# Performance work log

Measured on AMD Instinct MI355X. Metric: run time of the kernel, lower is better.

## Reference

```python
import jax, jax.numpy as jnp
import numpy as np

EPS = 1e-5
BN_GAMMA = 1.0
BN_BETA = 1e-4  # per torch init: BN weight=1, bias=0.0001


def bn(h):
    # BatchNorm1d in training mode: biased batch variance
    mu = h.mean(axis=0)
    var = h.var(axis=0)
    return (h - mu) * (BN_GAMMA / jnp.sqrt(var + EPS)) + BN_BETA


def gcn_conv(h, W, b, row, col, n, edge_weight=None):
    # PyG-style GCNConv: linear -> add self loops (w=1) -> sym deg norm -> scatter-sum
    h = h @ W
    e = row.shape[0]
    ew = jnp.ones((e,), h.dtype) if edge_weight is None else edge_weight
    loop = jnp.arange(n, dtype=row.dtype)
    r = jnp.concatenate([row, loop])
    c = jnp.concatenate([col, loop])
    w = jnp.concatenate([ew, jnp.ones((n,), h.dtype)])
    deg = jax.ops.segment_sum(w, r, num_segments=n)
    dinv = jnp.where(deg > 0, jax.lax.rsqrt(deg + jnp.where(deg > 0, 0.0, 1.0)), 0.0)
    norm = dinv[r] * w * dinv[c]  # [E+N]
    msg = h[r] * norm[:, None]    # gather + per-edge scale
    out = jax.ops.segment_sum(msg, c, num_segments=n)  # scatter-aggregate
    return out + b


def readout(h, W1, b1, W2, b2):
    h = bn(h) @ W1 + b1
    h = bn(jax.nn.relu(h)) @ W2 + b2
    return jax.nn.log_softmax(h, axis=-1)


def setup_inputs() -> dict:
    key = jax.random.key(0)
    ks = jax.random.split(key, 12)
    N, E, F, H, C = 50000, 800000, 128, 128, 10
    s = 0.05
    return {
        "x": jax.random.normal(ks[0], (N, F), jnp.float32),
        "edge_index": jax.random.randint(ks[1], (2, E), 0, N, jnp.int32),
        "perm": jax.random.permutation(ks[2], N).astype(jnp.int32),
        "W_feat": jax.random.normal(ks[3], (F, H), jnp.float32) * s,
        "b_feat": jnp.zeros((H,), jnp.float32),
        "W_convs": jax.random.normal(ks[4], (3, H, H), jnp.float32) * s,
        "b_convs": jnp.zeros((3, H), jnp.float32),
        "W_ea": jax.random.normal(ks[5], (2 * H, 2), jnp.float32) * s,
        "b_ea": jnp.zeros((2,), jnp.float32),
        "W_na": jax.random.normal(ks[6], (H, 2), jnp.float32) * s,
        "b_na": jnp.zeros((2,), jnp.float32),
        "W_ctx": jax.random.normal(ks[7], (H, H), jnp.float32) * s,
        "b_ctx": jnp.zeros((H,), jnp.float32),
        "W_obj": jax.random.normal(ks[8], (H, H), jnp.float32) * s,
        "b_obj": jnp.zeros((H,), jnp.float32),
        "W_fc1": jax.random.normal(ks[9], (3, H, H), jnp.float32) * s,  # c,o,co
        "b_fc1": jnp.zeros((3, H), jnp.float32),
        "W_fc2": jax.random.normal(ks[10], (3, H, C), jnp.float32) * s,
        "b_fc2": jnp.zeros((3, C), jnp.float32),
    }


def reference(x, edge_index, perm, W_feat, b_feat, W_convs, b_convs, W_ea, b_ea,
              W_na, b_na, W_ctx, b_ctx, W_obj, b_obj, W_fc1, b_fc1, W_fc2, b_fc2):
    n = x.shape[0]
    row, col = edge_index[0], edge_index[1]
    h = bn(x)
    h = jax.nn.relu(h @ W_feat + b_feat)  # conv_feat has gfn=True -> pure linear
    for i in range(3):
        h = jax.nn.relu(gcn_conv(bn(h), W_convs[i], b_convs[i], row, col, n))
    edge_rep = jnp.concatenate([h[row], h[col]], axis=-1)  # [E, 2H]
    edge_att = jax.nn.softmax(edge_rep @ W_ea + b_ea, axis=-1)
    node_att = jax.nn.softmax(h @ W_na + b_na, axis=-1)
    xc = node_att[:, 0:1] * h
    xo = node_att[:, 1:2] * h
    xc = jax.nn.relu(gcn_conv(bn(xc), W_ctx, b_ctx, row, col, n, edge_att[:, 0]))
    xo = jax.nn.relu(gcn_conv(bn(xo), W_obj, b_obj, row, col, n, edge_att[:, 1]))
    xc_logis = readout(xc, W_fc1[0], b_fc1[0], W_fc2[0], b_fc2[0])
    xo_logis = readout(xo, W_fc1[1], b_fc1[1], W_fc2[1], b_fc2[1])
    xco_logis = readout(xc[perm] + xo, W_fc1[2], b_fc1[2], W_fc2[2], b_fc2[2])
    return (xc_logis, xo_logis, xco_logis)
```

## Files before the change

kernel.cpp:

```cpp
#include <hip/hip_runtime.h>
#include <math.h>

#define H 128
#define NCLS 10
#define EPS 1e-5f
#define BN_BETA 1e-4f
#define CS_BLOCKS 256

typedef unsigned short u16;
typedef unsigned int u32;
typedef __attribute__((ext_vector_type(8))) short short8;
typedef __attribute__((ext_vector_type(4))) float floatx4;

__device__ inline float bflo(u32 u) { union { u32 i; float f; } a; a.i = u << 16; return a.f; }
__device__ inline float bfhi(u32 u) { union { u32 i; float f; } a; a.i = u & 0xffff0000u; return a.f; }
__device__ inline u16 f2bf(float f) {
  union { float f; u32 i; } v; v.f = f;
  return (u16)((v.i + 0x7fff + ((v.i >> 16) & 1)) >> 16);
}
__device__ inline u32 pack2(float a, float b) { return (u32)f2bf(a) | ((u32)f2bf(b) << 16); }

__device__ inline void reduce_partials(const float* __restrict__ P, int nb, int stride,
                                       int off0, int f, float* su_out, float* sq_out) {
  float su[8] = {0, 0, 0, 0, 0, 0, 0, 0}, sq[8] = {0, 0, 0, 0, 0, 0, 0, 0};
  int b = 0;
  for (; b + 8 <= nb; b += 8) {
#pragma unroll
    for (int u = 0; u < 8; u++) {
      const float* p = P + (size_t)(b + u) * stride + off0;
      su[u] += p[f];
      sq[u] += p[128 + f];
    }
  }
  for (; b < nb; b++) {
    const float* p = P + (size_t)b * stride + off0;
    su[0] += p[f];
    sq[0] += p[128 + f];
  }
  *su_out = ((su[0] + su[1]) + (su[2] + su[3])) + ((su[4] + su[5]) + (su[6] + su[7]));
  *sq_out = ((sq[0] + sq[1]) + (sq[2] + sq[3])) + ((sq[4] + sq[5]) + (sq[6] + sq[7]));
}

__global__ __launch_bounds__(256) void xstats_kernel(
    const float* __restrict__ x, int n4, float* __restrict__ stp) {
  int tid = threadIdx.x;
  int lane = tid & 63, wave = tid >> 6;
  float s[4] = {0, 0, 0, 0}, q[4] = {0, 0, 0, 0};
  int step = gridDim.x * 256;
  for (int i = blockIdx.x * 256 + tid; i < n4; i += step) {
    float4 v = ((const float4*)x)[i];
    s[0] += v.x; q[0] += v.x * v.x; s[1] += v.y; q[1] += v.y * v.y;
    s[2] += v.z; q[2] += v.z * v.z; s[3] += v.w; q[3] += v.w * v.w;
  }
#pragma unroll
  for (int k = 0; k < 4; k++) { s[k] += __shfl_xor(s[k], 32); q[k] += __shfl_xor(q[k], 32); }
  __shared__ float sm[4][256];
  int col = (lane & 31) * 4;
  if (lane < 32) {
#pragma unroll
    for (int k = 0; k < 4; k++) { sm[wave][col + k] = s[k]; sm[wave][128 + col + k] = q[k]; }
  }
  __syncthreads();
  stp[(size_t)blockIdx.x * 256 + tid] = sm[0][tid] + sm[1][tid] + sm[2][tid] + sm[3][tid];
}

__global__ __launch_bounds__(256) void colstats_kernel(
    const u16* __restrict__ X, int N, float* __restrict__ stp) {
  int tid = threadIdx.x;
  int li = tid & 15, rg = tid >> 4;
  int wave = tid >> 6, lane = tid & 63;
  const uint4* T = (const uint4*)X;
  float s[8] = {0, 0, 0, 0, 0, 0, 0, 0}, q[8] = {0, 0, 0, 0, 0, 0, 0, 0};
  for (int r = blockIdx.x * 16 + rg; r < N; r += CS_BLOCKS * 16) {
    uint4 u = T[(size_t)r * 16 + li];
    float f[8] = {bflo(u.x), bfhi(u.x), bflo(u.y), bfhi(u.y),
                  bflo(u.z), bfhi(u.z), bflo(u.w), bfhi(u.w)};
#pragma unroll
    for (int j = 0; j < 8; j++) { s[j] += f[j]; q[j] += f[j] * f[j]; }
  }
#pragma unroll
  for (int j = 0; j < 8; j++) {
    s[j] += __shfl_xor(s[j], 16); s[j] += __shfl_xor(s[j], 32);
    q[j] += __shfl_xor(q[j], 16); q[j] += __shfl_xor(q[j], 32);
  }
  __shared__ float sm[4][256];
  if ((lane & 48) == 0) {
#pragma unroll
    for (int j = 0; j < 8; j++) {
      sm[wave][li * 8 + j] = s[j];
      sm[wave][128 + li * 8 + j] = q[j];
    }
  }
  __syncthreads();
  stp[(size_t)blockIdx.x * 256 + tid] = sm[0][tid] + sm[1][tid] + sm[2][tid] + sm[3][tid];
}

__device__ inline void fold_body(const float* P, int nb, int stride, int off0,
                                 const float* W, const float* bias,
                                 float invN, int k, u16* Wt, float* cf) {
  int f = threadIdx.x;
  float su, sq;
  reduce_partials(P, nb, stride, off0, f, &su, &sq);
  float mu = su * invN;
  float var = sq * invN - mu * mu;
  float s = 1.0f / sqrtf(fmaxf(var, 0.f) + EPS);
  float w = W[(size_t)f * H + k];
  Wt[(size_t)k * H + f] = f2bf(s * w);
  __shared__ float red[H];
  red[f] = (BN_BETA - mu * s) * w;
  __syncthreads();
  for (int o = 64; o > 0; o >>= 1) {
    if (f < o) red[f] += red[f + o];
    __syncthreads();
  }
  if (f == 0) cf[k] = red[0] + (bias ? bias[k] : 0.f);
}

__global__ __launch_bounds__(128) void fold_kernel(
    const float* P, int nb, const float* W, const float* bias, float invN,
    u16* Wt, float* cf) {
  fold_body(P, nb, 256, 0, W, bias, invN, blockIdx.x, Wt, cf);
}

__global__ __launch_bounds__(128) void fold2_kernel(
    const float* P, int nb, const float* W0, const float* W1, float invN,
    u16* Wt2, float* cf2) {
  int j = blockIdx.x >> 7, k = blockIdx.x & 127;
  fold_body(P, nb, 512, j * 256, j ? W1 : W0, nullptr, invN, k,
            Wt2 + (size_t)j * H * H, cf2 + j * H);
}

__global__ __launch_bounds__(128) void fold3_kernel(
    const float* PC, int nbC, const float* PO, int nbO, const float* PCO, int nbCO,
    const float* W_fc1, const float* b_fc1, float invN, u16* Wt3, float* cf3) {
  int j = blockIdx.x >> 7, k = blockIdx.x & 127;
  const float* P = (j == 0) ? PC : (j == 1) ? PO : PCO;
  int nb = (j == 0) ? nbC : (j == 1) ? nbO : nbCO;
  fold_body(P, nb, 256, 0, W_fc1 + (size_t)j * H * H, b_fc1 + j * H, invN, k,
            Wt3 + (size_t)j * H * H, cf3 + j * H);
}

__global__ __launch_bounds__(128) void fold10x3_kernel(
    const float* stpZ, int nb, const float* W_fc2, const float* b_fc2, float invN,
    float* W2f, float* c2f) {
  int j = blockIdx.x / NCLS, k = blockIdx.x % NCLS;
  const float* P = stpZ + (size_t)j * nb * 256;
  int f = threadIdx.x;
  float su, sq;
  reduce_partials(P, nb, 256, 0, f, &su, &sq);
  float mu = su * invN;
  float var = sq * invN - mu * mu;
  float s = 1.0f / sqrtf(fmaxf(var, 0.f) + EPS);
  float w = W_fc2[(size_t)j * H * NCLS + (size_t)f * NCLS + k];
  W2f[(size_t)j * H * NCLS + (size_t)f * NCLS + k] = s * w;
  __shared__ float red[H];
  red[f] = (BN_BETA - mu * s) * w;
  __syncthreads();
  for (int o = 64; o > 0; o >>= 1) {
    if (f < o) red[f] += red[f + o];
    __syncthreads();
  }
  if (f == 0) c2f[j * 16 + k] = red[0] + b_fc2[j * NCLS + k];
}

__device__ inline void gemm_core(const u16* A, const float* Afp, const u16* Bt,
                                 const float* cf, const float* b2, const float* sumw,
                                 u16* C, int N, int relu, int blk, float* stp) {
  int tid = threadIdx.x;
  int wave = tid >> 6, lane = tid & 63;
  int l15 = lane & 15, quad = lane >> 4;
  int row0 = (blk * 4 + wave) * 16;
  if (row0 >= N && !stp) return;
  int arow = row0 + l15;
  short8 a[4];
  short8 z8 = {0, 0, 0, 0, 0, 0, 0, 0};
  if (Afp) {
#pragma unroll
    for (int k4 = 0; k4 < 4; k4++) {
      if (arow < N) {
        const float* p = Afp + (size_t)arow * H + k4 * 32 + quad * 8;
        float4 f0 = *(const float4*)p;
        float4 f1 = *(const float4*)(p + 4);
        union { short8 s8; u32 u[4]; } cv;
        cv.u[0] = pack2(f0.x, f0.y); cv.u[1] = pack2(f0.z, f0.w);
        cv.u[2] = pack2(f1.x, f1.y); cv.u[3] = pack2(f1.z, f1.w);
        a[k4] = cv.s8;
      } else a[k4] = z8;
    }
  } else {
#pragma unroll
    for (int k4 = 0; k4 < 4; k4++)
      a[k4] = (arow < N) ? *(const short8*)(A + (size_t)arow * H + k4 * 32 + quad * 8) : z8;
  }
  float srow[4];
  if (sumw) {
#pragma unroll
    for (int r = 0; r < 4; r++) {
      int row = row0 + quad * 4 + r;
      srow[r] = (row < N) ? sumw[row] : 0.f;
    }
  }
  float ps[8], pq[8];
#pragma unroll
  for (int nt = 0; nt < 8; nt++) {
    floatx4 acc = {0.f, 0.f, 0.f, 0.f};
    const u16* bp = Bt + (size_t)(nt * 16 + l15) * H + quad * 8;
#pragma unroll
    for (int k4 = 0; k4 < 4; k4++) {
      short8 b = *(const short8*)(bp + k4 * 32);
      acc = __builtin_amdgcn_mfma_f32_16x16x32_bf16(a[k4], b, acc, 0, 0, 0);
    }
    int col = nt * 16 + l15;
    float base = cf[col];
    float bb = b2 ? b2[col] : 0.f;
    float s_ = 0.f, q_ = 0.f;
#pragma unroll
    for (int r = 0; r < 4; r++) {
      int row = row0 + quad * 4 + r;
      if (row < N) {
        float v = acc[r] + (sumw ? srow[r] * base + bb : base);
        if (relu) v = fmaxf(v, 0.f);
        s_ += v; q_ += v * v;
        C[(size_t)row * H + col] = f2bf(v);
      }
    }
    ps[nt] = s_; pq[nt] = q_;
  }
  if (stp) {
    __shared__ float sred[4][256];
#pragma unroll
    for (int nt = 0; nt < 8; nt++) {
      ps[nt] += __shfl_xor(ps[nt], 16); ps[nt] += __shfl_xor(ps[nt], 32);
      pq[nt] += __shfl_xor(pq[nt], 16); pq[nt] += __shfl_xor(pq[nt], 32);
    }
    if (quad == 0) {
#pragma unroll
      for (int nt = 0; nt < 8; nt++) {
        sred[wave][nt * 16 + l15] = ps[nt];
        sred[wave][128 + nt * 16 + l15] = pq[nt];
      }
    }
    __syncthreads();
    stp[(size_t)blk * 256 + tid] =
        sred[0][tid] + sred[1][tid] + sred[2][tid] + sred[3][tid];
  }
}

__global__ __launch_bounds__(256) void gemm_kernel(
    const u16* A, const u16* Bt, const float* cf, u16* C, int N, int relu) {
  gemm_core(A, nullptr, Bt, cf, nullptr, nullptr, C, N, relu, blockIdx.x, nullptr);
}

__global__ __launch_bounds__(256) void gemm_x_kernel(
    const float* x, const u16* Bt, const float* cf, u16* C, int N, float* stp) {
  gemm_core(nullptr, x, Bt, cf, nullptr, nullptr, C, N, 1, blockIdx.x, stp);
}

__global__ __launch_bounds__(256) void gemm2sw_kernel(
    u16* B0, u16* B1, const u16* Wt2, const float* cf2,
    const float* b0, const float* b1, const float* sw0, const float* sw1,
    int N, int gG, float* stp) {
  int j = blockIdx.x / gG, blk = blockIdx.x % gG;
  u16* Z = j ? B1 : B0;
  gemm_core(Z, nullptr, Wt2 + (size_t)j * H * H, cf2 + j * H, j ? b1 : b0,
            j ? sw1 : sw0, Z, N, 1, blk, stp + (size_t)j * gG * 256);
}

__global__ __launch_bounds__(256) void gemm3_kernel(
    u16* Z0, u16* Z1, u16* Z2, const u16* Wt3, const float* cf3,
    int N, int gG, float* stp) {
  int j = blockIdx.x / gG, blk = blockIdx.x % gG;
  u16* Z = (j == 0) ? Z0 : (j == 1) ? Z1 : Z2;
  gemm_core(Z, nullptr, Wt3 + (size_t)j * H * H, cf3 + j * H, nullptr, nullptr,
            Z, N, 1, blk, stp + (size_t)j * gG * 256);
}

__global__ __launch_bounds__(256) void hist_kernel(
    const int* __restrict__ row, const int* __restrict__ col, int E,
    int* __restrict__ cnt, float* __restrict__ deg) {
  int e = blockIdx.x * 256 + threadIdx.x;
  if (e < E) {
    atomicAdd(&cnt[col[e]], 1);
    atomicAdd(&deg[row[e]], 1.0f);
  }
}

__global__ __launch_bounds__(256) void scanA_rsqrt_kernel(
    const int* __restrict__ cnt, const float* __restrict__ deg, int N,
    int* __restrict__ partial, float* __restrict__ dinv) {
  int i = blockIdx.x * 256 + threadIdx.x;
  if (i < N) dinv[i] = 1.0f / sqrtf(deg[i] + 1.0f);
  __shared__ int sd[256];
  sd[threadIdx.x] = (i < N) ? cnt[i] : 0;
  __syncthreads();
  for (int o = 128; o > 0; o >>= 1) {
    if (threadIdx.x < o) sd[threadIdx.x] += sd[threadIdx.x + o];
    __syncthreads();
  }
  if (threadIdx.x == 0) partial[blockIdx.x] = sd[0];
}

__global__ __launch_bounds__(256) void scanB_kernel(const int* __restrict__ partial, int nb,
                                                    int* __restrict__ blockoff) {
  __shared__ int sd[256];
  int t = threadIdx.x;
  int v = (t < nb) ? partial[t] : 0;
  sd[t] = v;
  __syncthreads();
  for (int o = 1; o < 256; o <<= 1) {
    int x = (t >= o) ? sd[t - o] : 0;
    __syncthreads();
    sd[t] += x;
    __syncthreads();
  }
  blockoff[t] = sd[t] - v;
}

__global__ __launch_bounds__(256) void scanC_kernel(
    const int* __restrict__ cnt, int N, const int* __restrict__ blockoff,
    int* __restrict__ off, int* __restrict__ cur, int E) {
  __shared__ int sd[256];
  int t = threadIdx.x;
  int i = blockIdx.x * 256 + t;
  int v = (i < N) ? cnt[i] : 0;
  sd[t] = v;
  __syncthreads();
  for (int o = 1; o < 256; o <<= 1) {
    int x = (t >= o) ? sd[t - o] : 0;
    __syncthreads();
    sd[t] += x;
    __syncthreads();
  }
  if (i < N) {
    int ex = blockoff[blockIdx.x] + sd[t] - v;
    off[i] = ex;
    cur[i] = ex;
  }
  if (i == 0) off[N] = E;
}

__global__ __launch_bounds__(256) void place_kernel(
    const int* __restrict__ row, const int* __restrict__ col, int E,
    int* __restrict__ cur, const float* __restrict__ dinv,
    int* __restrict__ csr_src, int* __restrict__ slot_of, float* __restrict__ wn) {
  int e = blockIdx.x * 256 + threadIdx.x;
  if (e < E) {
    int r = row[e];
    int slot = atomicAdd(&cur[col[e]], 1);
    csr_src[slot] = r;
    slot_of[e] = slot;
    wn[slot] = dinv[r];
  }
}

__global__ __launch_bounds__(256) void rsqrt2_kernel(
    const float* __restrict__ deg, const float* __restrict__ degc,
    float* __restrict__ dinvc, float* __restrict__ dinvo, int N) {
  int v = blockIdx.x * 256 + threadIdx.x;
  if (v < N) {
    float dc = degc[v];
    dinvc[v] = 1.0f / sqrtf(dc + 1.0f);
    dinvo[v] = 1.0f / sqrtf(deg[v] - dc + 1.0f);
  }
}

__global__ __launch_bounds__(256) void wa2_kernel(
    const int* csr_src, float* att_and_wa0r, const float* dinvc, const float* dinvo,
    const float2* na01, float* wa0n, float* wa1n, float* wa1r, int E) {
  int i = blockIdx.x * 256 + threadIdx.x;
  if (i >= E) return;
  int s = csr_src[i];
  float a0 = att_and_wa0r[i];
  float2 na = na01[s];
  float r0 = a0 * dinvc[s];
  float r1 = (1.0f - a0) * dinvo[s];
  wa0n[i] = r0 * na.x;
  wa1n[i] = r1 * na.y;
  att_and_wa0r[i] = r0;
  wa1r[i] = r1;
}

#define ACC8(A, U, W)                                             \
  A[0] += (W) * bflo(U.x); A[1] += (W) * bfhi(U.x);               \
  A[2] += (W) * bflo(U.y); A[3] += (W) * bfhi(U.y);               \
  A[4] += (W) * bflo(U.z); A[5] += (W) * bfhi(U.z);               \
  A[6] += (W) * bflo(U.w); A[7] += (W) * bfhi(U.w);

__global__ __launch_bounds__(256) void agg_kernel(
    const u16* __restrict__ t, const int* __restrict__ csr_src,
    const float* __restrict__ wseg, const int* __restrict__ off,
    const float* __restrict__ dinv, const float* __restrict__ bias,
    u16* __restrict__ out, int N) {
  int v = blockIdx.x * 4 + (threadIdx.x >> 6);
  if (v >= N) return;
  int lane = threadIdx.x & 63;
  int g = lane >> 4, li = lane & 15;
  const uint4* T = (const uint4*)t;
  float dv = dinv[v];
  float acc[8] = {0.f, 0.f, 0.f, 0.f, 0.f, 0.f, 0.f, 0.f};
  if (g == 0) {
    uint4 u = T[(size_t)v * 16 + li];
    float w0 = dv * dv;
    ACC8(acc, u, w0)
  }
  int s0 = off[v], s1 = off[v + 1];
  for (int s = s0; s < s1; s += 32) {
    int ix[8]; float wv[8];
#pragma unroll
    for (int u = 0; u < 8; u++) {
      int e = s + g + u * 4;
      bool ok = e < s1;
      int e2 = ok ? e : s0;
      ix[u] = csr_src[e2];
      wv[u] = ok ? wseg[e2] : 0.f;
    }
    uint4 uu[8];
#pragma unroll
    for (int u = 0; u < 8; u++) uu[u] = T[(size_t)ix[u] * 16 + li];
#pragma unroll
    for (int u = 0; u < 8; u++) { float w = wv[u] * dv; ACC8(acc, uu[u], w) }
  }
#pragma unroll
  for (int j = 0; j < 8; j++) {
    acc[j] += __shfl_xor(acc[j], 16);
    acc[j] += __shfl_xor(acc[j], 32);
  }
  if (g == 0) {
    float o[8];
#pragma unroll
    for (int j = 0; j < 8; j++) o[j] = fmaxf(acc[j] + bias[li * 8 + j], 0.f);
    uint4 w4;
    w4.x = pack2(o[0], o[1]); w4.y = pack2(o[2], o[3]);
    w4.z = pack2(o[4], o[5]); w4.w = pack2(o[6], o[7]);
    ((uint4*)out)[(size_t)v * 16 + li] = w4;
  }
}

__global__ __launch_bounds__(256) void aggdual_kernel(
    const u16* __restrict__ h, const int* __restrict__ csr_src,
    const float* __restrict__ wa0n, const float* __restrict__ wa1n,
    const float* __restrict__ wa0r, const float* __restrict__ wa1r,
    const int* __restrict__ off, const float* __restrict__ dinvc,
    const float* __restrict__ dinvo, const float2* __restrict__ na01,
    u16* __restrict__ gc, u16* __restrict__ go,
    float* __restrict__ sumw_c, float* __restrict__ sumw_o, int N) {
  int v = blockIdx.x * 4 + (threadIdx.x >> 6);
  if (v >= N) return;
  int lane = threadIdx.x & 63;
  int g = lane >> 4, li = lane & 15;
  const uint4* T = (const uint4*)h;
  float dvc = dinvc[v], dvo = dinvo[v];
  float ac[8] = {0.f, 0.f, 0.f, 0.f, 0.f, 0.f, 0.f, 0.f};
  float ao[8] = {0.f, 0.f, 0.f, 0.f, 0.f, 0.f, 0.f, 0.f};
  float swc = 0.f, swo = 0.f;
  if (g == 0) {
    uint4 u = T[(size_t)v * 16 + li];
    float2 na = na01[v];
    float wc = dvc * dvc, wo = dvo * dvo;
    float wch = wc * na.x, woh = wo * na.y;
    ACC8(ac, u, wch)
    ACC8(ao, u, woh)
  }
  int s0 = off[v], s1 = off[v + 1];
  for (int s = s0; s < s1; s += 16) {
    int ix[4]; float w0n[4], w1n[4], w0r[4], w1r[4];
#pragma unroll
    for (int u = 0; u < 4; u++) {
      int e = s + g + u * 4;
      bool ok = e < s1;
      int e2 = ok ? e : s0;
      ix[u] = csr_src[e2];
      w0n[u] = ok ? wa0n[e2] : 0.f;
      w1n[u] = ok ? wa1n[e2] : 0.f;
      w0r[u] = ok ? wa0r[e2] : 0.f;
      w1r[u] = ok ? wa1r[e2] : 0.f;
    }
    uint4 uu[4];
#pragma unroll
    for (int u = 0; u < 4; u++) uu[u] = T[(size_t)ix[u] * 16 + li];
#pragma unroll
    for (int u = 0; u < 4; u++) {
      float wc = w0n[u] * dvc; ACC8(ac, uu[u], wc)
      float wo = w1n[u] * dvo; ACC8(ao, uu[u], wo)
      swc += w0r[u]; swo += w1r[u];
    }
  }
#pragma unroll
  for (int j = 0; j < 8; j++) {
    ac[j] += __shfl_xor(ac[j], 16); ac[j] += __shfl_xor(ac[j], 32);
    ao[j] += __shfl_xor(ao[j], 16); ao[j] += __shfl_xor(ao[j], 32);
  }
  swc += __shfl_xor(swc, 16); swc += __shfl_xor(swc, 32);
  swo += __shfl_xor(swo, 16); swo += __shfl_xor(swo, 32);
  if (g == 0) {
    uint4 wc4, wo4;
    wc4.x = pack2(ac[0], ac[1]); wc4.y = pack2(ac[2], ac[3]);
    wc4.z = pack2(ac[4], ac[5]); wc4.w = pack2(ac[6], ac[7]);
    wo4.x = pack2(ao[0], ao[1]); wo4.y = pack2(ao[2], ao[3]);
    wo4.z = pack2(ao[4], ao[5]); wo4.w = pack2(ao[6], ao[7]);
    ((uint4*)gc)[(size_t)v * 16 + li] = wc4;
    ((uint4*)go)[(size_t)v * 16 + li] = wo4;
    if (li == 0) {
      sumw_c[v] = dvc * swc + dvc * dvc;
      sumw_o[v] = dvo * swo + dvo * dvo;
    }
  }
}

__global__ __launch_bounds__(256) void natt_kernel(
    const u16* __restrict__ h, int N,
    const float* __restrict__ W_na, const float* __restrict__ b_na,
    const float* __restrict__ W_ea,
    float2* __restrict__ na01, float2* __restrict__ p01, float2* __restrict__ q01) {
  int n = blockIdx.x * 256 + threadIdx.x;
  if (n >= N) return;
  float sa0 = 0, sa1 = 0, sp0 = 0, sp1 = 0, sq0 = 0, sq1 = 0;
  const uint2* hr = (const uint2*)(h + (size_t)n * H);
  for (int c = 0; c < 32; c++) {
    uint2 u = hr[c];
    float v0 = bflo(u.x), v1 = bfhi(u.x), v2 = bflo(u.y), v3 = bfhi(u.y);
    int k = c * 4;
    sa0 += v0 * W_na[k * 2] + v1 * W_na[k * 2 + 2] + v2 * W_na[k * 2 + 4] + v3 * W_na[k * 2 + 6];
    sa1 += v0 * W_na[k * 2 + 1] + v1 * W_na[k * 2 + 3] + v2 * W_na[k * 2 + 5] + v3 * W_na[k * 2 + 7];
    sp0 += v0 * W_ea[k * 2] + v1 * W_ea[k * 2 + 2] + v2 * W_ea[k * 2 + 4] + v3 * W_ea[k * 2 + 6];
    sp1 += v0 * W_ea[k * 2 + 1] + v1 * W_ea[k * 2 + 3] + v2 * W_ea[k * 2 + 5] + v3 * W_ea[k * 2 + 7];
    sq0 += v0 * W_ea[(H + k) * 2] + v1 * W_ea[(H + k) * 2 + 2] + v2 * W_ea[(H + k) * 2 + 4] + v3 * W_ea[(H + k) * 2 + 6];
    sq1 += v0 * W_ea[(H + k) * 2 + 1] + v1 * W_ea[(H + k) * 2 + 3] + v2 * W_ea[(H + k) * 2 + 5] + v3 * W_ea[(H + k) * 2 + 7];
  }
  sa0 += b_na[0]; sa1 += b_na[1];
  float m = fmaxf(sa0, sa1);
  float e0 = expf(sa0 - m), e1 = expf(sa1 - m);
  float inv = 1.f / (e0 + e1);
  na01[n] = make_float2(e0 * inv, e1 * inv);
  p01[n] = make_float2(sp0, sp1);
  q01[n] = make_float2(sq0, sq1);
}

__global__ __launch_bounds__(256) void xprestats_kernel(
    const u16* __restrict__ h, const float2* __restrict__ na01, int n4,
    float* __restrict__ stp) {
  int tid = threadIdx.x;
  int lane = tid & 63, wave = tid >> 6;
  float sc[4] = {0, 0, 0, 0}, qc[4] = {0, 0, 0, 0};
  float so[4] = {0, 0, 0, 0}, qo[4] = {0, 0, 0, 0};
  int step = gridDim.x * 256;
  for (int i = blockIdx.x * 256 + tid; i < n4; i += step) {
    int n = i >> 5;
    uint2 u = ((const uint2*)h)[i];
    float v0 = bflo(u.x), v1 = bfhi(u.x), v2 = bflo(u.y), v3 = bfhi(u.y);
    float2 ab = na01[n];
    float a = ab.x, b = ab.y;
    float c0 = v0 * a, c1 = v1 * a, c2 = v2 * a, c3 = v3 * a;
    float o0 = v0 * b, o1 = v1 * b, o2 = v2 * b, o3 = v3 * b;
    sc[0] += c0; qc[0] += c0 * c0; sc[1] += c1; qc[1] += c1 * c1;
    sc[2] += c2; qc[2] += c2 * c2; sc[3] += c3; qc[3] += c3 * c3;
    so[0] += o0; qo[0] += o0 * o0; so[1] += o1; qo[1] += o1 * o1;
    so[2] += o2; qo[2] += o2 * o2; so[3] += o3; qo[3] += o3 * o3;
  }
#pragma unroll
  for (int k = 0; k < 4; k++) {
    sc[k] += __shfl_xor(sc[k], 32); qc[k] += __shfl_xor(qc[k], 32);
    so[k] += __shfl_xor(so[k], 32); qo[k] += __shfl_xor(qo[k], 32);
  }
  __shared__ float sm[4][512];
  int col = (lane & 31) * 4;
  if (lane < 32) {
#pragma unroll
    for (int k = 0; k < 4; k++) {
      sm[wave][col + k] = sc[k];
      sm[wave][128 + col + k] = qc[k];
      sm[wave][256 + col + k] = so[k];
      sm[wave][384 + col + k] = qo[k];
    }
  }
  __syncthreads();
  float r0 = sm[0][tid] + sm[1][tid] + sm[2][tid] + sm[3][tid];
  float r1 = sm[0][256 + tid] + sm[1][256 + tid] + sm[2][256 + tid] + sm[3][256 + tid];
  stp[(size_t)blockIdx.x * 512 + tid] = r0;
  stp[(size_t)blockIdx.x * 512 + 256 + tid] = r1;
}

__global__ __launch_bounds__(256) void eatt_kernel(
    const int* __restrict__ row, const int* __restrict__ col, int E,
    const float2* __restrict__ p01, const float2* __restrict__ q01,
    const float* __restrict__ b_ea, const int* __restrict__ slot_of,
    float* __restrict__ att0s, float* __restrict__ degc) {
  int e = blockIdx.x * 256 + threadIdx.x;
  if (e >= E) return;
  int r = row[e], c = col[e];
  float2 p = p01[r], q = q01[c];
  float l0 = p.x + q.x + b_ea[0];
  float l1 = p.y + q.y + b_ea[1];
  float a0 = 1.0f / (1.0f + expf(l1 - l0));
  att0s[slot_of[e]] = a0;
  atomicAdd(&degc[r], a0);
}

__global__ __launch_bounds__(256) void permadd_stats_kernel(
    const u16* __restrict__ xc, const u16* __restrict__ xo,
    const int* __restrict__ perm, u16* __restrict__ out, int n4, float* __restrict__ stp) {
  int tid = threadIdx.x;
  int lane = tid & 63, wave = tid >> 6;
  float s[4] = {0, 0, 0, 0}, q[4] = {0, 0, 0, 0};
  int step = gridDim.x * 256;
  for (int i = blockIdx.x * 256 + tid; i < n4; i += step) {
    int n = i >> 5, k = i & 31;
    int p = perm[n];
    uint2 a = ((const uint2*)xc)[(size_t)p * 32 + k];
    uint2 b = ((const uint2*)xo)[i];
    float f0 = bflo(a.x) + bflo(b.x), f1 = bfhi(a.x) + bfhi(b.x);
    float f2 = bflo(a.y) + bflo(b.y), f3 = bfhi(a.y) + bfhi(b.y);
    ((uint2*)out)[i] = make_uint2(pack2(f0, f1), pack2(f2, f3));
    s[0] += f0; q[0] += f0 * f0; s[1] += f1; q[1] += f1 * f1;
    s[2] += f2; q[2] += f2 * f2; s[3] += f3; q[3] += f3 * f3;
  }
#pragma unroll
  for (int k = 0; k < 4; k++) { s[k] += __shfl_xor(s[k], 32); q[k] += __shfl_xor(q[k], 32); }
  __shared__ float sm[4][256];
  int col = (lane & 31) * 4;
  if (lane < 32) {
#pragma unroll
    for (int k = 0; k < 4; k++) { sm[wave][col + k] = s[k]; sm[wave][128 + col + k] = q[k]; }
  }
  __syncthreads();
  stp[(size_t)blockIdx.x * 256 + tid] = sm[0][tid] + sm[1][tid] + sm[2][tid] + sm[3][tid];
}

__global__ __launch_bounds__(256) void fc2x3_kernel(
    const u16* __restrict__ z0, const u16* __restrict__ z1, const u16* __restrict__ z2,
    const float* __restrict__ W2f, const float* __restrict__ c2f,
    float* __restrict__ outp, int N, int gN) {
  int j = blockIdx.x / gN, blk = blockIdx.x % gN;
  int n = blk * 256 + threadIdx.x;
  if (n >= N) return;
  const u16* z = (j == 0) ? z0 : (j == 1) ? z1 : z2;
  const float* W2 = W2f + (size_t)j * H * NCLS;
  const float* c2 = c2f + j * 16;
  float* op = outp + (size_t)j * N * NCLS;
  float acc[NCLS];
#pragma unroll
  for (int c = 0; c < NCLS; c++) acc[c] = c2[c];
  const uint2* zr = (const uint2*)(z + (size_t)n * H);
  for (int c4 = 0; c4 < 32; c4++) {
    uint2 u = zr[c4];
    float v[4] = {bflo(u.x), bfhi(u.x), bflo(u.y), bfhi(u.y)};
    int k = c4 * 4;
#pragma unroll
    for (int jj = 0; jj < 4; jj++)
#pragma unroll
      for (int c = 0; c < NCLS; c++) acc[c] += v[jj] * W2[(k + jj) * NCLS + c];
  }
  float m = acc[0];
#pragma unroll
  for (int c = 1; c < NCLS; c++) m = fmaxf(m, acc[c]);
  float s = 0.f;
#pragma unroll
  for (int c = 0; c < NCLS; c++) s += expf(acc[c] - m);
  float lse = logf(s) + m;
#pragma unroll
  for (int c = 0; c < NCLS; c++) op[(size_t)n * NCLS + c] = acc[c] - lse;
}

extern "C" void kernel_launch(void* const* d_in, const int* in_sizes, int n_in,
                              void* d_out, int out_size, void* d_ws, size_t ws_size,
                              hipStream_t stream) {
  const int N = in_sizes[0] / H;
  const int E = in_sizes[1] / 2;
  const float* x = (const float*)d_in[0];
  const int* ei = (const int*)d_in[1];
  const int* row = ei;
  const int* col = ei + E;
  const int* perm = (const int*)d_in[2];
  const float* W_feat = (const float*)d_in[3];
  const float* b_feat = (const float*)d_in[4];
  const float* W_convs = (const float*)d_in[5];
  const float* b_convs = (const float*)d_in[6];
  const float* W_ea = (const float*)d_in[7];
  const float* b_ea = (const float*)d_in[8];
  const float* W_na = (const float*)d_in[9];
  const float* b_na = (const float*)d_in[10];
  const float* W_ctx = (const float*)d_in[11];
  const float* b_ctx = (const float*)d_in[12];
  const float* W_obj = (const float*)d_in[13];
  const float* b_obj = (const float*)d_in[14];
  const float* W_fc1 = (const float*)d_in[15];
  const float* b_fc1 = (const float*)d_in[16];
  const float* W_fc2 = (const float*)d_in[17];
  const float* b_fc2 = (const float*)d_in[18];
  float* out = (float*)d_out;

  const int gG = (N + 63) / 64;
  const int gN = (N + 255) / 256;
  const int gE = (E + 255) / 256;
  const int SB = (N + 255) / 256;
  const int n4 = N * 32;
  const int gAgg = (N + 3) / 4;
  const float invN = 1.0f / (float)N;

  char* base = (char*)d_ws;
  size_t off_b = 0;
  auto alloc = [&](size_t bytes) -> void* {
    void* p = base + off_b;
    off_b = (off_b + bytes + 255) & ~(size_t)255;
    return p;
  };
  size_t NB2 = (size_t)N * H * sizeof(u16);
  u16* bufA = (u16*)alloc(NB2);
  u16* bufB = (u16*)alloc(NB2);
  u16* bufC = (u16*)alloc(NB2);
  u16* bufD = (u16*)alloc(NB2);
  int* cnt = (int*)alloc(3 * (size_t)N * 4);
  float* deg = (float*)(cnt + N);
  float* degc = (float*)(cnt + 2 * (size_t)N);
  float* stpX = (float*)alloc((size_t)CS_BLOCKS * 256 * 4);
  float* stpG = (float*)alloc(3 * (size_t)gG * 256 * 4);
  float* stpPre = (float*)alloc((size_t)CS_BLOCKS * 512 * 4);
  float* stpCO = (float*)alloc((size_t)CS_BLOCKS * 256 * 4);
  int* off = (int*)alloc(((size_t)N + 1) * 4);
  int* cur = (int*)alloc((size_t)N * 4);
  float* dinv = (float*)alloc((size_t)N * 4);
  float* dinvc = (float*)alloc((size_t)N * 4);
  float* dinvo = (float*)alloc((size_t)N * 4);
  float* sumw_c = (float*)alloc((size_t)N * 4);
  float* sumw_o = (float*)alloc((size_t)N * 4);
  float2* na01 = (float2*)alloc((size_t)N * 8);
  float2* p01 = (float2*)alloc((size_t)N * 8);
  float2* q01 = (float2*)alloc((size_t)N * 8);
  int* partial = (int*)alloc(256 * 4);
  int* blockoff = (int*)alloc(256 * 4);
  u16* Wt = (u16*)alloc((size_t)H * H * 2);
  u16* Wt2 = (u16*)alloc(2 * (size_t)H * H * 2);
  u16* Wt3 = (u16*)alloc(3 * (size_t)H * H * 2);
  float* cf = (float*)alloc(H * 4);
  float* cf2 = (float*)alloc(2 * H * 4);
  float* cf3 = (float*)alloc(3 * H * 4);
  float* W2f = (float*)alloc(3 * (size_t)H * NCLS * 4);
  float* c2f = (float*)alloc(3 * 16 * 4);
  int* csr_src = (int*)alloc((size_t)E * 4);
  int* slot_of = (int*)alloc((size_t)E * 4);
  float* att0s = (float*)alloc((size_t)E * 4);
  float* wn = (float*)alloc((size_t)E * 4);
  float* waX = (float*)alloc((size_t)E * 4);
  float* wa0n = (float*)slot_of;
  float* wa1n = wn;
  float* wa0r = att0s;
  float* wa1r = waX;

  hipMemsetAsync(cnt, 0, 3 * (size_t)N * 4, stream);

  hist_kernel<<<gE, 256, 0, stream>>>(row, col, E, cnt, deg);
  scanA_rsqrt_kernel<<<SB, 256, 0, stream>>>(cnt, deg, N, partial, dinv);
  scanB_kernel<<<1, 256, 0, stream>>>(partial, SB, blockoff);
  scanC_kernel<<<SB, 256, 0, stream>>>(cnt, N, blockoff, off, cur, E);
  place_kernel<<<gE, 256, 0, stream>>>(row, col, E, cur, dinv, csr_src, slot_of, wn);

  xstats_kernel<<<CS_BLOCKS, 256, 0, stream>>>(x, n4, stpX);
  fold_kernel<<<H, H, 0, stream>>>(stpX, CS_BLOCKS, W_feat, b_feat, invN, Wt, cf);
  gemm_x_kernel<<<gG, 256, 0, stream>>>(x, Wt, cf, bufA, N, stpG);

  const float* stprev = stpG;
  int nbprev = gG;
  for (int i = 0; i < 3; ++i) {
    fold_kernel<<<H, H, 0, stream>>>(stprev, nbprev, W_convs + (size_t)i * H * H,
                                     nullptr, invN, Wt, cf);
    gemm_kernel<<<gG, 256, 0, stream>>>(bufA, Wt, cf, bufB, N, 0);
    agg_kernel<<<gAgg, 256, 0, stream>>>(bufB, csr_src, wn, off, dinv,
                                         b_convs + (size_t)i * H, bufA, N);
    if (i < 2) {
      colstats_kernel<<<CS_BLOCKS, 256, 0, stream>>>(bufA, N, stpX);
      stprev = stpX; nbprev = CS_BLOCKS;
    }
  }

  natt_kernel<<<gN, 256, 0, stream>>>(bufA, N, W_na, b_na, W_ea, na01, p01, q01);
  eatt_kernel<<<gE, 256, 0, stream>>>(row, col, E, p01, q01, b_ea, slot_of, att0s, degc);
  rsqrt2_kernel<<<gN, 256, 0, stream>>>(deg, degc, dinvc, dinvo, N);
  wa2_kernel<<<gE, 256, 0, stream>>>(csr_src, att0s, dinvc, dinvo, na01,
                                     wa0n, wa1n, wa1r, E);
  xprestats_kernel<<<CS_BLOCKS, 256, 0, stream>>>(bufA, na01, n4, stpPre);

  fold2_kernel<<<2 * H, H, 0, stream>>>(stpPre, CS_BLOCKS, W_ctx, W_obj, invN, Wt2, cf2);
  aggdual_kernel<<<gAgg, 256, 0, stream>>>(bufA, csr_src, wa0n, wa1n, wa0r, wa1r,
                                           off, dinvc, dinvo, na01, bufC, bufD,
                                           sumw_c, sumw_o, N);
  gemm2sw_kernel<<<2 * gG, 256, 0, stream>>>(bufC, bufD, Wt2, cf2, b_ctx, b_obj,
                                             sumw_c, sumw_o, N, gG, stpG);

  permadd_stats_kernel<<<CS_BLOCKS, 256, 0, stream>>>(bufC, bufD, perm, bufA, n4, stpCO);

  fold3_kernel<<<3 * H, H, 0, stream>>>(stpG, gG, stpG + (size_t)gG * 256, gG,
                                        stpCO, CS_BLOCKS, W_fc1, b_fc1, invN, Wt3, cf3);
  gemm3_kernel<<<3 * gG, 256, 0, stream>>>(bufC, bufD, bufA, Wt3, cf3, N, gG, stpG);
  fold10x3_kernel<<<3 * NCLS, H, 0, stream>>>(stpG, gG, W_fc2, b_fc2, invN, W2f, c2f);
  fc2x3_kernel<<<3 * gN, 256, 0, stream>>>(bufC, bufD, bufA, W2f, c2f, out, N, gN);
}
```

Measured before the change: 920.0 us.

## Fuse independent small kernels into combined launches and fold rsqrt into edge weights

Pairs independent kernels (hist+xstats, scanA+fold, scanB+gemm_x, scanC+fold, place+gemm, eatt+xprestats, wa2+fold2) into single launches that split work by block index. This cuts the number of serial kernel launches and the idle gaps between dependent stages. The fold kernels now handle two output columns per 256-thread block. The rsqrt2 kernel is removed: wa2 computes the attention-degree normalisation inline and writes packed float2 weights for aggdual. The risk is heterogeneous blocks in one grid causing load imbalance, and extra edge-sized buffers.

```diff
diff --git a/kernel.cpp b/kernel.cpp
--- a/kernel.cpp
+++ b/kernel.cpp
@@ -41,64 +41,12 @@
   *sq_out = ((sq[0] + sq[1]) + (sq[2] + sq[3])) + ((sq[4] + sq[5]) + (sq[6] + sq[7]));
 }
 
-__global__ __launch_bounds__(256) void xstats_kernel(
-    const float* __restrict__ x, int n4, float* __restrict__ stp) {
-  int tid = threadIdx.x;
-  int lane = tid & 63, wave = tid >> 6;
-  float s[4] = {0, 0, 0, 0}, q[4] = {0, 0, 0, 0};
-  int step = gridDim.x * 256;
-  for (int i = blockIdx.x * 256 + tid; i < n4; i += step) {
-    float4 v = ((const float4*)x)[i];
-    s[0] += v.x; q[0] += v.x * v.x; s[1] += v.y; q[1] += v.y * v.y;
-    s[2] += v.z; q[2] += v.z * v.z; s[3] += v.w; q[3] += v.w * v.w;
-  }
-#pragma unroll
-  for (int k = 0; k < 4; k++) { s[k] += __shfl_xor(s[k], 32); q[k] += __shfl_xor(q[k], 32); }
-  __shared__ float sm[4][256];
-  int col = (lane & 31) * 4;
-  if (lane < 32) {
-#pragma unroll
-    for (int k = 0; k < 4; k++) { sm[wave][col + k] = s[k]; sm[wave][128 + col + k] = q[k]; }
-  }
-  __syncthreads();
-  stp[(size_t)blockIdx.x * 256 + tid] = sm[0][tid] + sm[1][tid] + sm[2][tid] + sm[3][tid];
-}
-
-__global__ __launch_bounds__(256) void colstats_kernel(
-    const u16* __restrict__ X, int N, float* __restrict__ stp) {
-  int tid = threadIdx.x;
-  int li = tid & 15, rg = tid >> 4;
-  int wave = tid >> 6, lane = tid & 63;
-  const uint4* T = (const uint4*)X;
-  float s[8] = {0, 0, 0, 0, 0, 0, 0, 0}, q[8] = {0, 0, 0, 0, 0, 0, 0, 0};
-  for (int r = blockIdx.x * 16 + rg; r < N; r += CS_BLOCKS * 16) {
-    uint4 u = T[(size_t)r * 16 + li];
-    float f[8] = {bflo(u.x), bfhi(u.x), bflo(u.y), bfhi(u.y),
-                  bflo(u.z), bfhi(u.z), bflo(u.w), bfhi(u.w)};
-#pragma unroll
-    for (int j = 0; j < 8; j++) { s[j] += f[j]; q[j] += f[j] * f[j]; }
-  }
-#pragma unroll
-  for (int j = 0; j < 8; j++) {
-    s[j] += __shfl_xor(s[j], 16); s[j] += __shfl_xor(s[j], 32);
-    q[j] += __shfl_xor(q[j], 16); q[j] += __shfl_xor(q[j], 32);
-  }
-  __shared__ float sm[4][256];
-  if ((lane & 48) == 0) {
-#pragma unroll
-    for (int j = 0; j < 8; j++) {
-      sm[wave][li * 8 + j] = s[j];
-      sm[wave][128 + li * 8 + j] = q[j];
-    }
-  }
-  __syncthreads();
-  stp[(size_t)blockIdx.x * 256 + tid] = sm[0][tid] + sm[1][tid] + sm[2][tid] + sm[3][tid];
-}
-
-__device__ inline void fold_body(const float* P, int nb, int stride, int off0,
-                                 const float* W, const float* bias,
-                                 float invN, int k, u16* Wt, float* cf) {
-  int f = threadIdx.x;
+__device__ inline void fold256_body(const float* P, int nb, int stride, int off0,
+                                    const float* W, const float* bias, float invN,
+                                    int kp, u16* Wt, float* cf) {
+  int f = threadIdx.x & 127;
+  int half = threadIdx.x >> 7;
+  int k = kp * 2 + half;
   float su, sq;
   reduce_partials(P, nb, stride, off0, f, &su, &sq);
   float mu = su * invN;
@@ -106,38 +54,351 @@
   float s = 1.0f / sqrtf(fmaxf(var, 0.f) + EPS);
   float w = W[(size_t)f * H + k];
   Wt[(size_t)k * H + f] = f2bf(s * w);
-  __shared__ float red[H];
-  red[f] = (BN_BETA - mu * s) * w;
+  __shared__ float red[2][128];
+  red[half][f] = (BN_BETA - mu * s) * w;
   __syncthreads();
   for (int o = 64; o > 0; o >>= 1) {
-    if (f < o) red[f] += red[f + o];
+    if (f < o) red[half][f] += red[half][f + o];
     __syncthreads();
   }
-  if (f == 0) cf[k] = red[0] + (bias ? bias[k] : 0.f);
-}
-
-__global__ __launch_bounds__(128) void fold_kernel(
+  if (f == 0) cf[k] = red[half][0] + (bias ? bias[k] : 0.f);
+}
+
+__device__ inline void hist_body(const int* __restrict__ row, const int* __restrict__ col,
+                                 int E, int* cnt, float* deg, int blk) {
+  int e = blk * 256 + threadIdx.x;
+  if (e < E) {
+    atomicAdd(&cnt[col[e]], 1);
+    atomicAdd(&deg[row[e]], 1.0f);
+  }
+}
+
+__device__ inline void xstats_body(const float* __restrict__ x, int n4,
+                                   float* __restrict__ stp, int blk) {
+  int tid = threadIdx.x;
+  int lane = tid & 63, wave = tid >> 6;
+  float s[4] = {0, 0, 0, 0}, q[4] = {0, 0, 0, 0};
+  int step = CS_BLOCKS * 256;
+  for (int i = blk * 256 + tid; i < n4; i += step) {
+    float4 v = ((const float4*)x)[i];
+    s[0] += v.x; q[0] += v.x * v.x; s[1] += v.y; q[1] += v.y * v.y;
+    s[2] += v.z; q[2] += v.z * v.z; s[3] += v.w; q[3] += v.w * v.w;
+  }
+#pragma unroll
+  for (int k = 0; k < 4; k++) { s[k] += __shfl_xor(s[k], 32); q[k] += __shfl_xor(q[k], 32); }
+  __shared__ float smx[4][256];
+  int col = (lane & 31) * 4;
+  if (lane < 32) {
+#pragma unroll
+    for (int k = 0; k < 4; k++) { smx[wave][col + k] = s[k]; smx[wave][128 + col + k] = q[k]; }
+  }
+  __syncthreads();
+  stp[(size_t)blk * 256 + tid] = smx[0][tid] + smx[1][tid] + smx[2][tid] + smx[3][tid];
+}
+
+__device__ inline void scanA_body(const int* cnt, const float* deg, int N,
+                                  int* partial, float* dinv, float* degc, int blk) {
+  int i = blk * 256 + threadIdx.x;
+  if (i < N) {
+    dinv[i] = 1.0f / sqrtf(deg[i] + 1.0f);
+    degc[i] = 0.f;
+  }
+  __shared__ int sdA[256];
+  sdA[threadIdx.x] = (i < N) ? cnt[i] : 0;
+  __syncthreads();
+  for (int o = 128; o > 0; o >>= 1) {
+    if (threadIdx.x < o) sdA[threadIdx.x] += sdA[threadIdx.x + o];
+    __syncthreads();
+  }
+  if (threadIdx.x == 0) partial[blk] = sdA[0];
+}
+
+__device__ inline void scanB_body(const int* partial, int nb, int* blockoff) {
+  __shared__ int sdB[256];
+  int t = threadIdx.x;
+  int v = (t < nb) ? partial[t] : 0;
+  sdB[t] = v;
+  __syncthreads();
+  for (int o = 1; o < 256; o <<= 1) {
+    int x = (t >= o) ? sdB[t - o] : 0;
+    __syncthreads();
+    sdB[t] += x;
+    __syncthreads();
+  }
+  blockoff[t] = sdB[t] - v;
+}
+
+__device__ inline void scanC_body(const int* cnt, int N, const int* blockoff,
+                                  int* off, int* cur, int E, int blk) {
+  __shared__ int sdC[256];
+  int t = threadIdx.x;
+  int i = blk * 256 + t;
+  int v = (i < N) ? cnt[i] : 0;
+  sdC[t] = v;
+  __syncthreads();
+  for (int o = 1; o < 256; o <<= 1) {
+    int x = (t >= o) ? sdC[t - o] : 0;
+    __syncthreads();
+    sdC[t] += x;
+    __syncthreads();
+  }
+  if (i < N) {
+    int ex = blockoff[blk] + sdC[t] - v;
+    off[i] = ex;
+    cur[i] = ex;
+  }
+  if (i == 0) off[N] = E;
+}
+
+__device__ inline void place_body(const int* row, const int* col, int E, int* cur,
+                                  const float* dinv, int* csr_src, int* slot_of,
+                                  float* wn, int blk) {
+  int e = blk * 256 + threadIdx.x;
+  if (e < E) {
+    int r = row[e];
+    int slot = atomicAdd(&cur[col[e]], 1);
+    csr_src[slot] = r;
+    slot_of[e] = slot;
+    wn[slot] = dinv[r];
+  }
+}
+
+__device__ inline void eatt_body(const int* row, const int* col, int E,
+                                 const float2* p01, const float2* q01,
+                                 const float* b_ea, const int* slot_of,
+                                 float* att0s, float* degc, int blk) {
+  int e = blk * 256 + threadIdx.x;
+  if (e >= E) return;
+  int r = row[e], c = col[e];
+  float2 p = p01[r], q = q01[c];
+  float l0 = p.x + q.x + b_ea[0];
+  float l1 = p.y + q.y + b_ea[1];
+  float a0 = 1.0f / (1.0f + expf(l1 - l0));
+  att0s[slot_of[e]] = a0;
+  atomicAdd(&degc[r], a0);
+}
+
+__device__ inline void xprestats_body(const u16* __restrict__ h,
+                                      const float2* __restrict__ na01, int n4,
+                                      float* __restrict__ stp, int blk) {
+  int tid = threadIdx.x;
+  int lane = tid & 63, wave = tid >> 6;
+  float sc[4] = {0, 0, 0, 0}, qc[4] = {0, 0, 0, 0};
+  float so[4] = {0, 0, 0, 0}, qo[4] = {0, 0, 0, 0};
+  int step = CS_BLOCKS * 256;
+  for (int i = blk * 256 + tid; i < n4; i += step) {
+    int n = i >> 5;
+    uint2 u = ((const uint2*)h)[i];
+    float v0 = bflo(u.x), v1 = bfhi(u.x), v2 = bflo(u.y), v3 = bfhi(u.y);
+    float2 ab = na01[n];
+    float a = ab.x, b = ab.y;
+    float c0 = v0 * a, c1 = v1 * a, c2 = v2 * a, c3 = v3 * a;
+    float o0 = v0 * b, o1 = v1 * b, o2 = v2 * b, o3 = v3 * b;
+    sc[0] += c0; qc[0] += c0 * c0; sc[1] += c1; qc[1] += c1 * c1;
+    sc[2] += c2; qc[2] += c2 * c2; sc[3] += c3; qc[3] += c3 * c3;
+    so[0] += o0; qo[0] += o0 * o0; so[1] += o1; qo[1] += o1 * o1;
+    so[2] += o2; qo[2] += o2 * o2; so[3] += o3; qo[3] += o3 * o3;
+  }
+#pragma unroll
+  for (int k = 0; k < 4; k++) {
+    sc[k] += __shfl_xor(sc[k], 32); qc[k] += __shfl_xor(qc[k], 32);
+    so[k] += __shfl_xor(so[k], 32); qo[k] += __shfl_xor(qo[k], 32);
+  }
+  __shared__ float smp[4][512];
+  int col = (lane & 31) * 4;
+  if (lane < 32) {
+#pragma unroll
+    for (int k = 0; k < 4; k++) {
+      smp[wave][col + k] = sc[k];
+      smp[wave][128 + col + k] = qc[k];
+      smp[wave][256 + col + k] = so[k];
+      smp[wave][384 + col + k] = qo[k];
+    }
+  }
+  __syncthreads();
+  float r0 = smp[0][tid] + smp[1][tid] + smp[2][tid] + smp[3][tid];
+  float r1 = smp[0][256 + tid] + smp[1][256 + tid] + smp[2][256 + tid] + smp[3][256 + tid];
+  stp[(size_t)blk * 512 + tid] = r0;
+  stp[(size_t)blk * 512 + 256 + tid] = r1;
+}
+
+__device__ inline void wa2_body(const int* csr_src, const float* att0s,
+                                const float* deg, const float* degc,
+                                const float2* na01, float2* wfa, float2* wfr,
+                                int E, int blk) {
+  int i = blk * 256 + threadIdx.x;
+  if (i >= E) return;
+  int s = csr_src[i];
+  float a0 = att0s[i];
+  float2 na = na01[s];
+  float dgc = degc[s];
+  float r0 = a0 / sqrtf(dgc + 1.0f);
+  float r1 = (1.0f - a0) / sqrtf(deg[s] - dgc + 1.0f);
+  wfa[i] = make_float2(r0 * na.x, r1 * na.y);
+  wfr[i] = make_float2(r0, r1);
+}
+
+__device__ inline void gemm_core(const u16* A, const float* Afp, const u16* Bt,
+                                 const float* cf, const float* b2, const float* sumw,
+                                 u16* C, int N, int relu, int blk, float* stp) {
+  int tid = threadIdx.x;
+  int wave = tid >> 6, lane = tid & 63;
+  int l15 = lane & 15, quad = lane >> 4;
+  int row0 = (blk * 4 + wave) * 16;
+  if (row0 >= N && !stp) return;
+  int arow = row0 + l15;
+  short8 a[4];
+  short8 z8 = {0, 0, 0, 0, 0, 0, 0, 0};
+  if (Afp) {
+#pragma unroll
+    for (int k4 = 0; k4 < 4; k4++) {
+      if (arow < N) {
+        const float* p = Afp + (size_t)arow * H + k4 * 32 + quad * 8;
+        float4 f0 = *(const float4*)p;
+        float4 f1 = *(const float4*)(p + 4);
+        union { short8 s8; u32 u[4]; } cv;
+        cv.u[0] = pack2(f0.x, f0.y); cv.u[1] = pack2(f0.z, f0.w);
+        cv.u[2] = pack2(f1.x, f1.y); cv.u[3] = pack2(f1.z, f1.w);
+        a[k4] = cv.s8;
+      } else a[k4] = z8;
+    }
+  } else {
+#pragma unroll
+    for (int k4 = 0; k4 < 4; k4++)
+      a[k4] = (arow < N) ? *(const short8*)(A + (size_t)arow * H + k4 * 32 + quad * 8) : z8;
+  }
+  float srow[4];
+  if (sumw) {
+#pragma unroll
+    for (int r = 0; r < 4; r++) {
+      int row = row0 + quad * 4 + r;
+      srow[r] = (row < N) ? sumw[row] : 0.f;
+    }
+  }
+  float ps[8], pq[8];
+#pragma unroll
+  for (int nt = 0; nt < 8; nt++) {
+    floatx4 acc = {0.f, 0.f, 0.f, 0.f};
+    const u16* bp = Bt + (size_t)(nt * 16 + l15) * H + quad * 8;
+#pragma unroll
+    for (int k4 = 0; k4 < 4; k4++) {
+      short8 b = *(const short8*)(bp + k4 * 32);
+      acc = __builtin_amdgcn_mfma_f32_16x16x32_bf16(a[k4], b, acc, 0, 0, 0);
+    }
+    int col = nt * 16 + l15;
+    float base = cf[col];
+    float bb = b2 ? b2[col] : 0.f;
+    float s_ = 0.f, q_ = 0.f;
+#pragma unroll
+    for (int r = 0; r < 4; r++) {
+      int row = row0 + quad * 4 + r;
+      if (row < N) {
+        float v = acc[r] + (sumw ? srow[r] * base + bb : base);
+        if (relu) v = fmaxf(v, 0.f);
+        s_ += v; q_ += v * v;
+        C[(size_t)row * H + col] = f2bf(v);
+      }
+    }
+    ps[nt] = s_; pq[nt] = q_;
+  }
+  if (stp) {
+    __shared__ float sred[4][256];
+#pragma unroll
+    for (int nt = 0; nt < 8; nt++) {
+      ps[nt] += __shfl_xor(ps[nt], 16); ps[nt] += __shfl_xor(ps[nt], 32);
+      pq[nt] += __shfl_xor(pq[nt], 16); pq[nt] += __shfl_xor(pq[nt], 32);
+    }
+    if (quad == 0) {
+#pragma unroll
+      for (int nt = 0; nt < 8; nt++) {
+        sred[wave][nt * 16 + l15] = ps[nt];
+        sred[wave][128 + nt * 16 + l15] = pq[nt];
+      }
+    }
+    __syncthreads();
+    stp[(size_t)blk * 256 + tid] =
+        sred[0][tid] + sred[1][tid] + sred[2][tid] + sred[3][tid];
+  }
+}
+
+__global__ __launch_bounds__(256) void hist_xstats_kernel(
+    const int* row, const int* col, int E, int* cnt, float* deg, int gE,
+    const float* x, int n4, float* stpX) {
+  if ((int)blockIdx.x < gE) hist_body(row, col, E, cnt, deg, blockIdx.x);
+  else xstats_body(x, n4, stpX, blockIdx.x - gE);
+}
+
+__global__ __launch_bounds__(256) void scanA_fold_kernel(
+    const int* cnt, const float* deg, int N, int* partial, float* dinv, float* degc,
+    int SB, const float* stpX, const float* W_feat, const float* b_feat, float invN,
+    u16* WtA, float* cfA) {
+  if ((int)blockIdx.x < SB) scanA_body(cnt, deg, N, partial, dinv, degc, blockIdx.x);
+  else fold256_body(stpX, CS_BLOCKS, 256, 0, W_feat, b_feat, invN, blockIdx.x - SB, WtA, cfA);
+}
+
+__global__ __launch_bounds__(256) void scanB_gemmx_kernel(
+    const int* partial, int nb, int* blockoff,
+    const float* x, const u16* WtA, const float* cfA, u16* C, int N, float* stpG) {
+  if (blockIdx.x == 0) scanB_body(partial, nb, blockoff);
+  else gemm_core(nullptr, x, WtA, cfA, nullptr, nullptr, C, N, 1, blockIdx.x - 1, stpG);
+}
+
+__global__ __launch_bounds__(256) void scanC_fold_kernel(
+    const int* cnt, int N, const int* blockoff, int* off, int* cur, int E, int SB,
+    const float* stpG, int nbG, const float* Wc, float invN, u16* WtB, float* cfB) {
+  if ((int)blockIdx.x < SB) scanC_body(cnt, N, blockoff, off, cur, E, blockIdx.x);
+  else fold256_body(stpG, nbG, 256, 0, Wc, nullptr, invN, blockIdx.x - SB, WtB, cfB);
+}
+
+__global__ __launch_bounds__(256) void place_gemm_kernel(
+    const int* row, const int* col, int E, int* cur, const float* dinv,
+    int* csr_src, int* slot_of, float* wn, int gE,
+    const u16* A, const u16* WtB, const float* cfB, u16* C, int N) {
+  if ((int)blockIdx.x < gE)
+    place_body(row, col, E, cur, dinv, csr_src, slot_of, wn, blockIdx.x);
+  else
+    gemm_core(A, nullptr, WtB, cfB, nullptr, nullptr, C, N, 0, blockIdx.x - gE, nullptr);
+}
+
+__global__ __launch_bounds__(256) void eatt_xpre_kernel(
+    const int* row, const int* col, int E, const float2* p01, const float2* q01,
+    const float* b_ea, const int* slot_of, float* att0s, float* degc, int gE,
+    const u16* h, const float2* na01, int n4, float* stpPre) {
+  if ((int)blockIdx.x < gE)
+    eatt_body(row, col, E, p01, q01, b_ea, slot_of, att0s, degc, blockIdx.x);
+  else
+    xprestats_body(h, na01, n4, stpPre, blockIdx.x - gE);
+}
+
+__global__ __launch_bounds__(256) void wa2_fold2_kernel(
+    const int* csr_src, const float* att0s, const float* deg, const float* degc,
+    const float2* na01, float2* wfa, float2* wfr, int E, int gE,
+    const float* stpPre, const float* W_ctx, const float* W_obj, float invN,
+    u16* Wt2, float* cf2) {
+  if ((int)blockIdx.x < gE)
+    wa2_body(csr_src, att0s, deg, degc, na01, wfa, wfr, E, blockIdx.x);
+  else {
+    int b = blockIdx.x - gE;
+    int j = b >> 6, kp = b & 63;
+    fold256_body(stpPre, CS_BLOCKS, 512, j * 256, j ? W_obj : W_ctx, nullptr, invN, kp,
+                 Wt2 + (size_t)j * H * H, cf2 + j * H);
+  }
+}
+
+__global__ __launch_bounds__(256) void fold256_kernel(
     const float* P, int nb, const float* W, const float* bias, float invN,
     u16* Wt, float* cf) {
-  fold_body(P, nb, 256, 0, W, bias, invN, blockIdx.x, Wt, cf);
-}
-
-__global__ __launch_bounds__(128) void fold2_kernel(
-    const float* P, int nb, const float* W0, const float* W1, float invN,
-    u16* Wt2, float* cf2) {
-  int j = blockIdx.x >> 7, k = blockIdx.x & 127;
-  fold_body(P, nb, 512, j * 256, j ? W1 : W0, nullptr, invN, k,
-            Wt2 + (size_t)j * H * H, cf2 + j * H);
-}
-
-__global__ __launch_bounds__(128) void fold3_kernel(
+  fold256_body(P, nb, 256, 0, W, bias, invN, blockIdx.x, Wt, cf);
+}
+
+__global__ __launch_bounds__(256) void fold3_kernel(
     const float* PC, int nbC, const float* PO, int nbO, const float* PCO, int nbCO,
     const float* W_fc1, const float* b_fc1, float invN, u16* Wt3, float* cf3) {
-  int j = blockIdx.x >> 7, k = blockIdx.x & 127;
+  int j = blockIdx.x / 64, kp = blockIdx.x % 64;
   const float* P = (j == 0) ? PC : (j == 1) ? PO : PCO;
   int nb = (j == 0) ? nbC : (j == 1) ? nbO : nbCO;
-  fold_body(P, nb, 256, 0, W_fc1 + (size_t)j * H * H, b_fc1 + j * H, invN, k,
-            Wt3 + (size_t)j * H * H, cf3 + j * H);
+  fold256_body(P, nb, 256, 0, W_fc1 + (size_t)j * H * H, b_fc1 + j * H, invN, kp,
+               Wt3 + (size_t)j * H * H, cf3 + j * H);
 }
 
 __global__ __launch_bounds__(128) void fold10x3_kernel(
@@ -153,107 +414,19 @@
   float s = 1.0f / sqrtf(fmaxf(var, 0.f) + EPS);
   float w = W_fc2[(size_t)j * H * NCLS + (size_t)f * NCLS + k];
   W2f[(size_t)j * H * NCLS + (size_t)f * NCLS + k] = s * w;
-  __shared__ float red[H];
-  red[f] = (BN_BETA - mu * s) * w;
+  __shared__ float red1[H];
+  red1[f] = (BN_BETA - mu * s) * w;
   __syncthreads();
   for (int o = 64; o > 0; o >>= 1) {
-    if (f < o) red[f] += red[f + o];
+    if (f < o) red1[f] += red1[f + o];
     __syncthreads();
   }
-  if (f == 0) c2f[j * 16 + k] = red[0] + b_fc2[j * NCLS + k];
-}
-
-__device__ inline void gemm_core(const u16* A, const float* Afp, const u16* Bt,
-                                 const float* cf, const float* b2, const float* sumw,
-                                 u16* C, int N, int relu, int blk, float* stp) {
-  int tid = threadIdx.x;
-  int wave = tid >> 6, lane = tid & 63;
-  int l15 = lane & 15, quad = lane >> 4;
-  int row0 = (blk * 4 + wave) * 16;
-  if (row0 >= N && !stp) return;
-  int arow = row0 + l15;
-  short8 a[4];
-  short8 z8 = {0, 0, 0, 0, 0, 0, 0, 0};
-  if (Afp) {
-#pragma unroll
-    for (int k4 = 0; k4 < 4; k4++) {
-      if (arow < N) {
-        const float* p = Afp + (size_t)arow * H + k4 * 32 + quad * 8;
-        float4 f0 = *(const float4*)p;
-        float4 f1 = *(const float4*)(p + 4);
-        union { short8 s8; u32 u[4]; } cv;
-        cv.u[0] = pack2(f0.x, f0.y); cv.u[1] = pack2(f0.z, f0.w);
-        cv.u[2] = pack2(f1.x, f1.y); cv.u[3] = pack2(f1.z, f1.w);
-        a[k4] = cv.s8;
-      } else a[k4] = z8;
-    }
-  } else {
-#pragma unroll
-    for (int k4 = 0; k4 < 4; k4++)
-      a[k4] = (arow < N) ? *(const short8*)(A + (size_t)arow * H + k4 * 32 + quad * 8) : z8;
-  }
-  float srow[4];
-  if (sumw) {
-#pragma unroll
-    for (int r = 0; r < 4; r++) {
-      int row = row0 + quad * 4 + r;
-      srow[r] = (row < N) ? sumw[row] : 0.f;
-    }
-  }
-  float ps[8], pq[8];
-#pragma unroll
-  for (int nt = 0; nt < 8; nt++) {
-    floatx4 acc = {0.f, 0.f, 0.f, 0.f};
-    const u16* bp = Bt + (size_t)(nt * 16 + l15) * H + quad * 8;
-#pragma unroll
-    for (int k4 = 0; k4 < 4; k4++) {
-      short8 b = *(const short8*)(bp + k4 * 32);
-      acc = __builtin_amdgcn_mfma_f32_16x16x32_bf16(a[k4], b, acc, 0, 0, 0);
-    }
-    int col = nt * 16 + l15;
-    float base = cf[col];
-    float bb = b2 ? b2[col] : 0.f;
-    float s_ = 0.f, q_ = 0.f;
-#pragma unroll
-    for (int r = 0; r < 4; r++) {
-      int row = row0 + quad * 4 + r;
-      if (row < N) {
-        float v = acc[r] + (sumw ? srow[r] * base + bb : base);
-        if (relu) v = fmaxf(v, 0.f);
-        s_ += v; q_ += v * v;
-        C[(size_t)row * H + col] = f2bf(v);
-      }
-    }
-    ps[nt] = s_; pq[nt] = q_;
-  }
-  if (stp) {
-    __shared__ float sred[4][256];
-#pragma unroll
-    for (int nt = 0; nt < 8; nt++) {
-      ps[nt] += __shfl_xor(ps[nt], 16); ps[nt] += __shfl_xor(ps[nt], 32);
-      pq[nt] += __shfl_xor(pq[nt], 16); pq[nt] += __shfl_xor(pq[nt], 32);
-    }
-    if (quad == 0) {
-#pragma unroll
-      for (int nt = 0; nt < 8; nt++) {
-        sred[wave][nt * 16 + l15] = ps[nt];
-        sred[wave][128 + nt * 16 + l15] = pq[nt];
-      }
-    }
-    __syncthreads();
-    stp[(size_t)blk * 256 + tid] =
-        sred[0][tid] + sred[1][tid] + sred[2][tid] + sred[3][tid];
-  }
+  if (f == 0) c2f[j * 16 + k] = red1[0] + b_fc2[j * NCLS + k];
 }
 
 __global__ __launch_bounds__(256) void gemm_kernel(
     const u16* A, const u16* Bt, const float* cf, u16* C, int N, int relu) {
   gemm_core(A, nullptr, Bt, cf, nullptr, nullptr, C, N, relu, blockIdx.x, nullptr);
-}
-
-__global__ __launch_bounds__(256) void gemm_x_kernel(
-    const float* x, const u16* Bt, const float* cf, u16* C, int N, float* stp) {
-  gemm_core(nullptr, x, Bt, cf, nullptr, nullptr, C, N, 1, blockIdx.x, stp);
 }
 
 __global__ __launch_bounds__(256) void gemm2sw_kernel(
@@ -275,109 +448,35 @@
             Z, N, 1, blk, stp + (size_t)j * gG * 256);
 }
 
-__global__ __launch_bounds__(256) void hist_kernel(
-    const int* __restrict__ row, const int* __restrict__ col, int E,
-    int* __restrict__ cnt, float* __restrict__ deg) {
-  int e = blockIdx.x * 256 + threadIdx.x;
-  if (e < E) {
-    atomicAdd(&cnt[col[e]], 1);
-    atomicAdd(&deg[row[e]], 1.0f);
-  }
-}
-
-__global__ __launch_bounds__(256) void scanA_rsqrt_kernel(
-    const int* __restrict__ cnt, const float* __restrict__ deg, int N,
-    int* __restrict__ partial, float* __restrict__ dinv) {
-  int i = blockIdx.x * 256 + threadIdx.x;
-  if (i < N) dinv[i] = 1.0f / sqrtf(deg[i] + 1.0f);
-  __shared__ int sd[256];
-  sd[threadIdx.x] = (i < N) ? cnt[i] : 0;
+__global__ __launch_bounds__(256) void colstats_kernel(
+    const u16* __restrict__ X, int N, float* __restrict__ stp) {
+  int tid = threadIdx.x;
+  int li = tid & 15, rg = tid >> 4;
+  int wave = tid >> 6, lane = tid & 63;
+  const uint4* T = (const uint4*)X;
+  float s[8] = {0, 0, 0, 0, 0, 0, 0, 0}, q[8] = {0, 0, 0, 0, 0, 0, 0, 0};
+  for (int r = blockIdx.x * 16 + rg; r < N; r += CS_BLOCKS * 16) {
+    uint4 u = T[(size_t)r * 16 + li];
+    float f[8] = {bflo(u.x), bfhi(u.x), bflo(u.y), bfhi(u.y),
+                  bflo(u.z), bfhi(u.z), bflo(u.w), bfhi(u.w)};
+#pragma unroll
+    for (int j = 0; j < 8; j++) { s[j] += f[j]; q[j] += f[j] * f[j]; }
+  }
+#pragma unroll
+  for (int j = 0; j < 8; j++) {
+    s[j] += __shfl_xor(s[j], 16); s[j] += __shfl_xor(s[j], 32);
+    q[j] += __shfl_xor(q[j], 16); q[j] += __shfl_xor(q[j], 32);
+  }
+  __shared__ float smc[4][256];
+  if ((lane & 48) == 0) {
+#pragma unroll
+    for (int j = 0; j < 8; j++) {
+      smc[wave][li * 8 + j] = s[j];
+      smc[wave][128 + li * 8 + j] = q[j];
+    }
+  }
   __syncthreads();
-  for (int o = 128; o > 0; o >>= 1) {
-    if (threadIdx.x < o) sd[threadIdx.x] += sd[threadIdx.x + o];
-    __syncthreads();
-  }
-  if (threadIdx.x == 0) partial[blockIdx.x] = sd[0];
-}
-
-__global__ __launch_bounds__(256) void scanB_kernel(const int* __restrict__ partial, int nb,
-                                                    int* __restrict__ blockoff) {
-  __shared__ int sd[256];
-  int t = threadIdx.x;
-  int v = (t < nb) ? partial[t] : 0;
-  sd[t] = v;
-  __syncthreads();
-  for (int o = 1; o < 256; o <<= 1) {
-    int x = (t >= o) ? sd[t - o] : 0;
-    __syncthreads();
-    sd[t] += x;
-    __syncthreads();
-  }
-  blockoff[t] = sd[t] - v;
-}
-
-__global__ __launch_bounds__(256) void scanC_kernel(
-    const int* __restrict__ cnt, int N, const int* __restrict__ blockoff,
-    int* __restrict__ off, int* __restrict__ cur, int E) {
-  __shared__ int sd[256];
-  int t = threadIdx.x;
-  int i = blockIdx.x * 256 + t;
-  int v = (i < N) ? cnt[i] : 0;
-  sd[t] = v;
-  __syncthreads();
-  for (int o = 1; o < 256; o <<= 1) {
-    int x = (t >= o) ? sd[t - o] : 0;
-    __syncthreads();
-    sd[t] += x;
-    __syncthreads();
-  }
-  if (i < N) {
-    int ex = blockoff[blockIdx.x] + sd[t] - v;
-    off[i] = ex;
-    cur[i] = ex;
-  }
-  if (i == 0) off[N] = E;
-}
-
-__global__ __launch_bounds__(256) void place_kernel(
-    const int* __restrict__ row, const int* __restrict__ col, int E,
-    int* __restrict__ cur, const float* __restrict__ dinv,
-    int* __restrict__ csr_src, int* __restrict__ slot_of, float* __restrict__ wn) {
-  int e = blockIdx.x * 256 + threadIdx.x;
-  if (e < E) {
-    int r = row[e];
-    int slot = atomicAdd(&cur[col[e]], 1);
-    csr_src[slot] = r;
-    slot_of[e] = slot;
-    wn[slot] = dinv[r];
-  }
-}
-
-__global__ __launch_bounds__(256) void rsqrt2_kernel(
-    const float* __restrict__ deg, const float* __restrict__ degc,
-    float* __restrict__ dinvc, float* __restrict__ dinvo, int N) {
-  int v = blockIdx.x * 256 + threadIdx.x;
-  if (v < N) {
-    float dc = degc[v];
-    dinvc[v] = 1.0f / sqrtf(dc + 1.0f);
-    dinvo[v] = 1.0f / sqrtf(deg[v] - dc + 1.0f);
-  }
-}
-
-__global__ __launch_bounds__(256) void wa2_kernel(
-    const int* csr_src, float* att_and_wa0r, const float* dinvc, const float* dinvo,
-    const float2* na01, float* wa0n, float* wa1n, float* wa1r, int E) {
-  int i = blockIdx.x * 256 + threadIdx.x;
-  if (i >= E) return;
-  int s = csr_src[i];
-  float a0 = att_and_wa0r[i];
-  float2 na = na01[s];
-  float r0 = a0 * dinvc[s];
-  float r1 = (1.0f - a0) * dinvo[s];
-  wa0n[i] = r0 * na.x;
-  wa1n[i] = r1 * na.y;
-  att_and_wa0r[i] = r0;
-  wa1r[i] = r1;
+  stp[(size_t)blockIdx.x * 256 + tid] = smc[0][tid] + smc[1][tid] + smc[2][tid] + smc[3][tid];
 }
 
 #define ACC8(A, U, W)                                             \
@@ -438,10 +537,9 @@
 
 __global__ __launch_bounds__(256) void aggdual_kernel(
     const u16* __restrict__ h, const int* __restrict__ csr_src,
-    const float* __restrict__ wa0n, const float* __restrict__ wa1n,
-    const float* __restrict__ wa0r, const float* __restrict__ wa1r,
-    const int* __restrict__ off, const float* __restrict__ dinvc,
-    const float* __restrict__ dinvo, const float2* __restrict__ na01,
+    const float2* __restrict__ wfa, const float2* __restrict__ wfr,
+    const int* __restrict__ off, const float* __restrict__ deg,
+    const float* __restrict__ degc, const float2* __restrict__ na01,
     u16* __restrict__ gc, u16* __restrict__ go,
     float* __restrict__ sumw_c, float* __restrict__ sumw_o, int N) {
   int v = blockIdx.x * 4 + (threadIdx.x >> 6);
@@ -449,7 +547,9 @@
   int lane = threadIdx.x & 63;
   int g = lane >> 4, li = lane & 15;
   const uint4* T = (const uint4*)h;
-  float dvc = dinvc[v], dvo = dinvo[v];
+  float dgc = degc[v];
+  float dvc = 1.0f / sqrtf(dgc + 1.0f);
+  float dvo = 1.0f / sqrtf(deg[v] - dgc + 1.0f);
   float ac[8] = {0.f, 0.f, 0.f, 0.f, 0.f, 0.f, 0.f, 0.f};
   float ao[8] = {0.f, 0.f, 0.f, 0.f, 0.f, 0.f, 0.f, 0.f};
   float swc = 0.f, swo = 0.f;
@@ -463,26 +563,24 @@
   }
   int s0 = off[v], s1 = off[v + 1];
   for (int s = s0; s < s1; s += 16) {
-    int ix[4]; float w0n[4], w1n[4], w0r[4], w1r[4];
+    int ix[4]; float2 fa[4], fr[4];
 #pragma unroll
     for (int u = 0; u < 4; u++) {
       int e = s + g + u * 4;
       bool ok = e < s1;
       int e2 = ok ? e : s0;
       ix[u] = csr_src[e2];
-      w0n[u] = ok ? wa0n[e2] : 0.f;
-      w1n[u] = ok ? wa1n[e2] : 0.f;
-      w0r[u] = ok ? wa0r[e2] : 0.f;
-      w1r[u] = ok ? wa1r[e2] : 0.f;
+      fa[u] = ok ? wfa[e2] : make_float2(0.f, 0.f);
+      fr[u] = ok ? wfr[e2] : make_float2(0.f, 0.f);
     }
     uint4 uu[4];
 #pragma unroll
     for (int u = 0; u < 4; u++) uu[u] = T[(size_t)ix[u] * 16 + li];
 #pragma unroll
     for (int u = 0; u < 4; u++) {
-      float wc = w0n[u] * dvc; ACC8(ac, uu[u], wc)
-      float wo = w1n[u] * dvo; ACC8(ao, uu[u], wo)
-      swc += w0r[u]; swo += w1r[u];
+      float wc = fa[u].x * dvc; ACC8(ac, uu[u], wc)
+      float wo = fa[u].y * dvo; ACC8(ao, uu[u], wo)
+      swc += fr[u].x; swo += fr[u].y;
     }
   }
 #pragma unroll
@@ -536,73 +634,13 @@
   q01[n] = make_float2(sq0, sq1);
 }
 
-__global__ __launch_bounds__(256) void xprestats_kernel(
-    const u16* __restrict__ h, const float2* __restrict__ na01, int n4,
-    float* __restrict__ stp) {
-  int tid = threadIdx.x;
-  int lane = tid & 63, wave = tid >> 6;
-  float sc[4] = {0, 0, 0, 0}, qc[4] = {0, 0, 0, 0};
-  float so[4] = {0, 0, 0, 0}, qo[4] = {0, 0, 0, 0};
-  int step = gridDim.x * 256;
-  for (int i = blockIdx.x * 256 + tid; i < n4; i += step) {
-    int n = i >> 5;
-    uint2 u = ((const uint2*)h)[i];
-    float v0 = bflo(u.x), v1 = bfhi(u.x), v2 = bflo(u.y), v3 = bfhi(u.y);
-    float2 ab = na01[n];
-    float a = ab.x, b = ab.y;
-    float c0 = v0 * a, c1 = v1 * a, c2 = v2 * a, c3 = v3 * a;
-    float o0 = v0 * b, o1 = v1 * b, o2 = v2 * b, o3 = v3 * b;
-    sc[0] += c0; qc[0] += c0 * c0; sc[1] += c1; qc[1] += c1 * c1;
-    sc[2] += c2; qc[2] += c2 * c2; sc[3] += c3; qc[3] += c3 * c3;
-    so[0] += o0; qo[0] += o0 * o0; so[1] += o1; qo[1] += o1 * o1;
-    so[2] += o2; qo[2] += o2 * o2; so[3] += o3; qo[3] += o3 * o3;
-  }
-#pragma unroll
-  for (int k = 0; k < 4; k++) {
-    sc[k] += __shfl_xor(sc[k], 32); qc[k] += __shfl_xor(qc[k], 32);
-    so[k] += __shfl_xor(so[k], 32); qo[k] += __shfl_xor(qo[k], 32);
-  }
-  __shared__ float sm[4][512];
-  int col = (lane & 31) * 4;
-  if (lane < 32) {
-#pragma unroll
-    for (int k = 0; k < 4; k++) {
-      sm[wave][col + k] = sc[k];
-      sm[wave][128 + col + k] = qc[k];
-      sm[wave][256 + col + k] = so[k];
-      sm[wave][384 + col + k] = qo[k];
-    }
-  }
-  __syncthreads();
-  float r0 = sm[0][tid] + sm[1][tid] + sm[2][tid] + sm[3][tid];
-  float r1 = sm[0][256 + tid] + sm[1][256 + tid] + sm[2][256 + tid] + sm[3][256 + tid];
-  stp[(size_t)blockIdx.x * 512 + tid] = r0;
-  stp[(size_t)blockIdx.x * 512 + 256 + tid] = r1;
-}
-
-__global__ __launch_bounds__(256) void eatt_kernel(
-    const int* __restrict__ row, const int* __restrict__ col, int E,
-    const float2* __restrict__ p01, const float2* __restrict__ q01,
-    const float* __restrict__ b_ea, const int* __restrict__ slot_of,
-    float* __restrict__ att0s, float* __restrict__ degc) {
-  int e = blockIdx.x * 256 + threadIdx.x;
-  if (e >= E) return;
-  int r = row[e], c = col[e];
-  float2 p = p01[r], q = q01[c];
-  float l0 = p.x + q.x + b_ea[0];
-  float l1 = p.y + q.y + b_ea[1];
-  float a0 = 1.0f / (1.0f + expf(l1 - l0));
-  att0s[slot_of[e]] = a0;
-  atomicAdd(&degc[r], a0);
-}
-
 __global__ __launch_bounds__(256) void permadd_stats_kernel(
     const u16* __restrict__ xc, const u16* __restrict__ xo,
     const int* __restrict__ perm, u16* __restrict__ out, int n4, float* __restrict__ stp) {
   int tid = threadIdx.x;
   int lane = tid & 63, wave = tid >> 6;
   float s[4] = {0, 0, 0, 0}, q[4] = {0, 0, 0, 0};
-  int step = gridDim.x * 256;
+  int step = CS_BLOCKS * 256;
   for (int i = blockIdx.x * 256 + tid; i < n4; i += step) {
     int n = i >> 5, k = i & 31;
     int p = perm[n];
@@ -616,14 +654,14 @@
   }
 #pragma unroll
   for (int k = 0; k < 4; k++) { s[k] += __shfl_xor(s[k], 32); q[k] += __shfl_xor(q[k], 32); }
-  __shared__ float sm[4][256];
+  __shared__ float smq[4][256];
   int col = (lane & 31) * 4;
   if (lane < 32) {
 #pragma unroll
-    for (int k = 0; k < 4; k++) { sm[wave][col + k] = s[k]; sm[wave][128 + col + k] = q[k]; }
+    for (int k = 0; k < 4; k++) { smq[wave][col + k] = s[k]; smq[wave][128 + col + k] = q[k]; }
   }
   __syncthreads();
-  stp[(size_t)blockIdx.x * 256 + tid] = sm[0][tid] + sm[1][tid] + sm[2][tid] + sm[3][tid];
+  stp[(size_t)blockIdx.x * 256 + tid] = smq[0][tid] + smq[1][tid] + smq[2][tid] + smq[3][tid];
 }
 
 __global__ __launch_bounds__(256) void fc2x3_kernel(
@@ -709,9 +747,9 @@
   u16* bufB = (u16*)alloc(NB2);
   u16* bufC = (u16*)alloc(NB2);
   u16* bufD = (u16*)alloc(NB2);
-  int* cnt = (int*)alloc(3 * (size_t)N * 4);
+  int* cnt = (int*)alloc(2 * (size_t)N * 4);
   float* deg = (float*)(cnt + N);
-  float* degc = (float*)(cnt + 2 * (size_t)N);
+  float* degc = (float*)alloc((size_t)N * 4);
   float* stpX = (float*)alloc((size_t)CS_BLOCKS * 256 * 4);
   float* stpG = (float*)alloc(3 * (size_t)gG * 256 * 4);
   float* stpPre = (float*)alloc((size_t)CS_BLOCKS * 512 * 4);
@@ -719,8 +757,6 @@
   int* off = (int*)alloc(((size_t)N + 1) * 4);
   int* cur = (int*)alloc((size_t)N * 4);
   float* dinv = (float*)alloc((size_t)N * 4);
-  float* dinvc = (float*)alloc((size_t)N * 4);
-  float* dinvo = (float*)alloc((size_t)N * 4);
   float* sumw_c = (float*)alloc((size_t)N * 4);
   float* sumw_o = (float*)alloc((size_t)N * 4);
   float2* na01 = (float2*)alloc((size_t)N * 8);
@@ -728,10 +764,12 @@
   float2* q01 = (float2*)alloc((size_t)N * 8);
   int* partial = (int*)alloc(256 * 4);
   int* blockoff = (int*)alloc(256 * 4);
-  u16* Wt = (u16*)alloc((size_t)H * H * 2);
+  u16* WtA = (u16*)alloc((size_t)H * H * 2);
+  u16* WtB = (u16*)alloc((size_t)H * H * 2);
   u16* Wt2 = (u16*)alloc(2 * (size_t)H * H * 2);
   u16* Wt3 = (u16*)alloc(3 * (size_t)H * H * 2);
-  float* cf = (float*)alloc(H * 4);
+  float* cfA = (float*)alloc(H * 4);
+  float* cfB = (float*)alloc(H * 4);
   float* cf2 = (float*)alloc(2 * H * 4);
   float* cf3 = (float*)alloc(3 * H * 4);
   float* W2f = (float*)alloc(3 * (size_t)H * NCLS * 4);
@@ -740,57 +778,50 @@
   int* slot_of = (int*)alloc((size_t)E * 4);
   float* att0s = (float*)alloc((size_t)E * 4);
   float* wn = (float*)alloc((size_t)E * 4);
-  float* waX = (float*)alloc((size_t)E * 4);
-  float* wa0n = (float*)slot_of;
-  float* wa1n = wn;
-  float* wa0r = att0s;
-  float* wa1r = waX;
-
-  hipMemsetAsync(cnt, 0, 3 * (size_t)N * 4, stream);
-
-  hist_kernel<<<gE, 256, 0, stream>>>(row, col, E, cnt, deg);
-  scanA_rsqrt_kernel<<<SB, 256, 0, stream>>>(cnt, deg, N, partial, dinv);
-  scanB_kernel<<<1, 256, 0, stream>>>(partial, SB, blockoff);
-  scanC_kernel<<<SB, 256, 0, stream>>>(cnt, N, blockoff, off, cur, E);
-  place_kernel<<<gE, 256, 0, stream>>>(row, col, E, cur, dinv, csr_src, slot_of, wn);
-
-  xstats_kernel<<<CS_BLOCKS, 256, 0, stream>>>(x, n4, stpX);
-  fold_kernel<<<H, H, 0, stream>>>(stpX, CS_BLOCKS, W_feat, b_feat, invN, Wt, cf);
-  gemm_x_kernel<<<gG, 256, 0, stream>>>(x, Wt, cf, bufA, N, stpG);
-
-  const float* stprev = stpG;
-  int nbprev = gG;
-  for (int i = 0; i < 3; ++i) {
-    fold_kernel<<<H, H, 0, stream>>>(stprev, nbprev, W_convs + (size_t)i * H * H,
-                                     nullptr, invN, Wt, cf);
-    gemm_kernel<<<gG, 256, 0, stream>>>(bufA, Wt, cf, bufB, N, 0);
+  float2* wfa = (float2*)alloc((size_t)E * 8);
+  float2* wfr = (float2*)alloc((size_t)E * 8);
+
+  hipMemsetAsync(cnt, 0, 2 * (size_t)N * 4, stream);
+
+  hist_xstats_kernel<<<gE + CS_BLOCKS, 256, 0, stream>>>(row, col, E, cnt, deg, gE,
+                                                         x, n4, stpX);
+  scanA_fold_kernel<<<SB + 64, 256, 0, stream>>>(cnt, deg, N, partial, dinv, degc, SB,
+                                                 stpX, W_feat, b_feat, invN, WtA, cfA);
+  scanB_gemmx_kernel<<<1 + gG, 256, 0, stream>>>(partial, SB, blockoff, x, WtA, cfA,
+                                                 bufA, N, stpG);
+  scanC_fold_kernel<<<SB + 64, 256, 0, stream>>>(cnt, N, blockoff, off, cur, E, SB,
+                                                 stpG, gG, W_convs, invN, WtB, cfB);
+  place_gemm_kernel<<<gE + gG, 256, 0, stream>>>(row, col, E, cur, dinv, csr_src,
+                                                 slot_of, wn, gE, bufA, WtB, cfB,
+                                                 bufB, N);
+  agg_kernel<<<gAgg, 256, 0, stream>>>(bufB, csr_src, wn, off, dinv, b_convs, bufA, N);
+
+  for (int i = 1; i < 3; ++i) {
+    colstats_kernel<<<CS_BLOCKS, 256, 0, stream>>>(bufA, N, stpX);
+    fold256_kernel<<<64, 256, 0, stream>>>(stpX, CS_BLOCKS, W_convs + (size_t)i * H * H,
+                                           nullptr, invN, WtB, cfB);
+    gemm_kernel<<<gG, 256, 0, stream>>>(bufA, WtB, cfB, bufB, N, 0);
     agg_kernel<<<gAgg, 256, 0, stream>>>(bufB, csr_src, wn, off, dinv,
                                          b_convs + (size_t)i * H, bufA, N);
-    if (i < 2) {
-      colstats_kernel<<<CS_BLOCKS, 256, 0, stream>>>(bufA, N, stpX);
-      stprev = stpX; nbprev = CS_BLOCKS;
-    }
   }
 
   natt_kernel<<<gN, 256, 0, stream>>>(bufA, N, W_na, b_na, W_ea, na01, p01, q01);
-  eatt_kernel<<<gE, 256, 0, stream>>>(row, col, E, p01, q01, b_ea, slot_of, att0s, degc);
-  rsqrt2_kernel<<<gN, 256, 0, stream>>>(deg, degc, dinvc, dinvo, N);
-  wa2_kernel<<<gE, 256, 0, stream>>>(csr_src, att0s, dinvc, dinvo, na01,
-                                     wa0n, wa1n, wa1r, E);
-  xprestats_kernel<<<CS_BLOCKS, 256, 0, stream>>>(bufA, na01, n4, stpPre);
-
-  fold2_kernel<<<2 * H, H, 0, stream>>>(stpPre, CS_BLOCKS, W_ctx, W_obj, invN, Wt2, cf2);
-  aggdual_kernel<<<gAgg, 256, 0, stream>>>(bufA, csr_src, wa0n, wa1n, wa0r, wa1r,
-                                           off, dinvc, dinvo, na01, bufC, bufD,
-                                           sumw_c, sumw_o, N);
+  eatt_xpre_kernel<<<gE + CS_BLOCKS, 256, 0, stream>>>(row, col, E, p01, q01, b_ea,
+                                                       slot_of, att0s, degc, gE,
+                                                       bufA, na01, n4, stpPre);
+  wa2_fold2_kernel<<<gE + 128, 256, 0, stream>>>(csr_src, att0s, deg, degc, na01,
+                                                 wfa, wfr, E, gE, stpPre, W_ctx,
+                                                 W_obj, invN, Wt2, cf2);
+  aggdual_kernel<<<gAgg, 256, 0, stream>>>(bufA, csr_src, wfa, wfr, off, deg, degc,
+                                           na01, bufC, bufD, sumw_c, sumw_o, N);
   gemm2sw_kernel<<<2 * gG, 256, 0, stream>>>(bufC, bufD, Wt2, cf2, b_ctx, b_obj,
                                              sumw_c, sumw_o, N, gG, stpG);
 
   permadd_stats_kernel<<<CS_BLOCKS, 256, 0, stream>>>(bufC, bufD, perm, bufA, n4, stpCO);
 
-  fold3_kernel<<<3 * H, H, 0, stream>>>(stpG, gG, stpG + (size_t)gG * 256, gG,
+  fold3_kernel<<<192, 256, 0, stream>>>(stpG, gG, stpG + (size_t)gG * 256, gG,
                                         stpCO, CS_BLOCKS, W_fc1, b_fc1, invN, Wt3, cf3);
   gemm3_kernel<<<3 * gG, 256, 0, stream>>>(bufC, bufD, bufA, Wt3, cf3, N, gG, stpG);
-  fold10x3_kernel<<<3 * NCLS, H, 0, stream>>>(stpG, gG, W_fc2, b_fc2, invN, W2f, c2f);
+  fold10x3_kernel<<<3 * NCLS, 128, 0, stream>>>(stpG, gG, W_fc2, b_fc2, invN, W2f, c2f);
   fc2x3_kernel<<<3 * gN, 256, 0, stream>>>(bufC, bufD, bufA, W2f, c2f, out, N, gN);
 }
```

Measured after the change: 904.5 us. Within noise of the previous version (-1.7%).
